# Optimization experiments

Hardware: AMD Instinct MI355X
Metric: run time of the kernel (lower is better)

## Reference

```python
import jax, jax.numpy as jnp
import numpy as np

B, T, H = 4, 4096, 1024


def setup_inputs() -> dict:
    key = jax.random.key(0)
    k1, k2 = jax.random.split(key)
    h = jax.random.normal(k1, (B, T, H), dtype=jnp.float32)
    # nn.Linear weight, scaled for stable magnitudes
    W = jax.random.normal(k2, (H, H), dtype=jnp.float32) / np.sqrt(H).astype(np.float32)
    return {"h": h, "W": W, "T_hist": 256}


def reference(h, W, T_hist):
    Bb, Tt, Hh = h.shape
    # K = Linear(h) = h @ W.T ; Q = V = h
    K = jnp.einsum('bth,oh->bto', h, W)
    scores = jnp.einsum('bqh,bkh->bqk', h, K) / jnp.sqrt(jnp.asarray(Hh, h.dtype))
    # banded mask: causal (j <= i) AND limited history (j >= i - (T_hist-1))
    i = jnp.arange(Tt)[:, None]
    j = jnp.arange(Tt)[None, :]
    valid = (j <= i) & (j >= i - (T_hist - 1))
    scores = jnp.where(valid[None, :, :], scores, -jnp.inf)
    attn = jax.nn.softmax(scores, axis=-1)
    attn = jnp.nan_to_num(attn, nan=0.0)  # matches torch nan_to_num(0.0)
    context = jnp.einsum('bqk,bkh->bqh', attn, h)
    return context
```

## Files before the change

### kernel.cpp

```cpp
#include <hip/hip_runtime.h>
#include <hip/hip_bf16.h>

#define B_ 4
#define T_ 4096
#define H_ 1024
#define WP2 320

typedef short  s16x8 __attribute__((ext_vector_type(8)));
typedef float  f32x4 __attribute__((ext_vector_type(4)));
typedef unsigned short u16;

static __device__ __forceinline__ u16 bf16rn(float f) {
  unsigned int u = __float_as_uint(f);
  u += 0x7fffu + ((u >> 16) & 1u);
  return (u16)(u >> 16);
}

static __device__ __forceinline__ void gl2lds16(const u16* g, u16* l) {
  __builtin_amdgcn_global_load_lds(
      (__attribute__((address_space(1))) void*)(g),
      (__attribute__((address_space(3))) void*)(l), 16, 0, 0);
}

__global__ __launch_bounds__(256) void k_convT(const float* __restrict__ h,
                                               u16* __restrict__ hb,
                                               u16* __restrict__ hbT) {
  __shared__ unsigned int tile32[64 * 33];
  const int b  = blockIdx.z;
  const int t0 = blockIdx.y * 64;
  const int c0 = blockIdx.x * 64;
  const int t  = threadIdx.x;
  {
    const int r  = t >> 2;
    const int cq = (t & 3) << 4;
    const size_t g = (size_t)(b * T_ + t0 + r) * H_ + c0 + cq;
    const f32x4* src = (const f32x4*)(h + g);
    u16 o[16];
#pragma unroll
    for (int v = 0; v < 4; ++v) {
      f32x4 x = src[v];
#pragma unroll
      for (int j = 0; j < 4; ++j) o[v * 4 + j] = bf16rn(x[j]);
    }
    s16x8 w0, w1;
#pragma unroll
    for (int j = 0; j < 8; ++j) { w0[j] = (short)o[j]; w1[j] = (short)o[8 + j]; }
    *(s16x8*)(hb + g)     = w0;
    *(s16x8*)(hb + g + 8) = w1;
#pragma unroll
    for (int i = 0; i < 8; ++i)
      tile32[r * 33 + (cq >> 1) + i] =
          (unsigned int)o[2 * i] | ((unsigned int)o[2 * i + 1] << 16);
  }
  __syncthreads();
  {
    const int fpair = t & 31;
    const int kq    = t >> 5;
    unsigned int v[8];
#pragma unroll
    for (int j = 0; j < 8; ++j) v[j] = tile32[(kq * 8 + j) * 33 + fpair];
    s16x8 w0, w1;
#pragma unroll
    for (int j = 0; j < 8; ++j) {
      w0[j] = (short)(v[j] & 0xffffu);
      w1[j] = (short)(v[j] >> 16);
    }
    const size_t o0 = (size_t)(b * H_ + c0 + 2 * fpair) * T_ + t0 + kq * 8;
    *(s16x8*)(hbT + o0)      = w0;
    *(s16x8*)(hbT + o0 + T_) = w1;
  }
}

__global__ __launch_bounds__(256) void k_convW(const float* __restrict__ src,
                                               u16* __restrict__ dst) {
  const int i = (blockIdx.x * 256 + threadIdx.x) * 8;
  f32x4 a = *(const f32x4*)(src + i);
  f32x4 b = *(const f32x4*)(src + i + 4);
  s16x8 w;
#pragma unroll
  for (int j = 0; j < 4; ++j) {
    w[j]     = (short)bf16rn(a[j]);
    w[4 + j] = (short)bf16rn(b[j]);
  }
  *(s16x8*)(dst + i) = w;
}

__global__ __launch_bounds__(256) void k_gemmK(const u16* __restrict__ hb,
                                               const u16* __restrict__ Wb,
                                               u16* __restrict__ Kb) {
  __shared__ __align__(16) u16 As[3][512 * 8];
  __shared__ __align__(16) u16 Bs[3][512 * 8];
  const int t = threadIdx.x;
  const int id  = blockIdx.y * gridDim.x + blockIdx.x;
  const int swz = (id & 7) * 128 + (id >> 3);
  const int row0 = (swz >> 3) * 128;
  const int col0 = (swz & 7) * 128;
  const int lane = t & 63, wv = t >> 6;
  const int wr = wv >> 1, wc = wv & 1;
  const int l15 = lane & 15, quad = lane >> 4;

  const int c0 = t, c1 = t + 256;
  const size_t gA0 = (size_t)(row0 + (c0 >> 2)) * H_ + (c0 & 3) * 8;
  const size_t gA1 = (size_t)(row0 + (c1 >> 2)) * H_ + (c1 & 3) * 8;
  const size_t gB0 = (size_t)(col0 + (c0 >> 2)) * H_ + (c0 & 3) * 8;
  const size_t gB1 = (size_t)(col0 + (c1 >> 2)) * H_ + (c1 & 3) * 8;

  f32x4 acc[4][4];
#pragma unroll
  for (int m = 0; m < 4; ++m)
#pragma unroll
    for (int n = 0; n < 4; ++n) acc[m][n] = (f32x4)0.0f;

  gl2lds16(hb + gA0, &As[0][c0 * 8]);
  gl2lds16(hb + gA1, &As[0][c1 * 8]);
  gl2lds16(Wb + gB0, &Bs[0][c0 * 8]);
  gl2lds16(Wb + gB1, &Bs[0][c1 * 8]);
  gl2lds16(hb + gA0 + 32, &As[1][c0 * 8]);
  gl2lds16(hb + gA1 + 32, &As[1][c1 * 8]);
  gl2lds16(Wb + gB0 + 32, &Bs[1][c0 * 8]);
  gl2lds16(Wb + gB1 + 32, &Bs[1][c1 * 8]);
  asm volatile("s_waitcnt vmcnt(4)" ::: "memory");
  __builtin_amdgcn_s_barrier();

#pragma unroll
  for (int kt = 0; kt < 32; ++kt) {
    if (kt + 2 < 32) {
      const int sn = (kt + 2) % 3;
      const int off = (kt + 2) * 32;
      gl2lds16(hb + gA0 + off, &As[sn][c0 * 8]);
      gl2lds16(hb + gA1 + off, &As[sn][c1 * 8]);
      gl2lds16(Wb + gB0 + off, &Bs[sn][c0 * 8]);
      gl2lds16(Wb + gB1 + off, &Bs[sn][c1 * 8]);
    }
    const int sc = kt % 3;
    s16x8 aF[4], bF[4];
#pragma unroll
    for (int mt = 0; mt < 4; ++mt)
      aF[mt] = *(const s16x8*)&As[sc][((wr * 64 + mt * 16 + l15) * 4 + quad) * 8];
#pragma unroll
    for (int nt = 0; nt < 4; ++nt)
      bF[nt] = *(const s16x8*)&Bs[sc][((wc * 64 + nt * 16 + l15) * 4 + quad) * 8];
#pragma unroll
    for (int mt = 0; mt < 4; ++mt)
#pragma unroll
      for (int nt = 0; nt < 4; ++nt)
        acc[mt][nt] = __builtin_amdgcn_mfma_f32_16x16x32_bf16(aF[mt], bF[nt],
                                                              acc[mt][nt], 0, 0, 0);
    if (kt + 1 < 32) {
      if (kt <= 29) asm volatile("s_waitcnt vmcnt(4)" ::: "memory");
      else          asm volatile("s_waitcnt vmcnt(0)" ::: "memory");
      __builtin_amdgcn_s_barrier();
    }
  }
#pragma unroll
  for (int mt = 0; mt < 4; ++mt)
#pragma unroll
    for (int nt = 0; nt < 4; ++nt)
#pragma unroll
      for (int r = 0; r < 4; ++r) {
        const int row = row0 + wr * 64 + mt * 16 + quad * 4 + r;
        const int col = col0 + wc * 64 + nt * 16 + l15;
        Kb[(size_t)row * H_ + col] = bf16rn(acc[mt][nt][r]);
      }
}

__global__ __launch_bounds__(512) void k_scores(const u16* __restrict__ hb,
                                                const u16* __restrict__ Kb,
                                                u16* __restrict__ P) {
  __shared__ __align__(16) u16 Ks[3][1280 * 8];
  __shared__ float Sred[2][4][16];
  const int t = threadIdx.x;
  const int wv = t >> 6, lane = t & 63;
  const int l15 = lane & 15, quad = lane >> 4;
  const int id  = blockIdx.x;
  const int swz = (id & 7) * 64 + (id >> 3);
  const int b  = swz >> 7;
  const int q0 = (swz & 127) * 32;
  const int qt = wv & 1;
  const int sub = wv >> 1;
  const int qt0 = q0 + qt * 16;
  const int ktbase = (sub == 0) ? 0 : (1 + sub * 4);
  const int nkt = (sub == 0) ? 5 : 4;

  const u16* st[3];
  int cid[3];
#pragma unroll
  for (int p = 0; p < 3; ++p) {
    int c = p * 512 + t;
    if (c > 1279) c = 1279;
    cid[p] = c;
    if (c < 1152) {
      const int m = c >> 6, lr = (c >> 2) & 15, qd = c & 3;
      int tok = q0 - 256 + m * 16 + lr;
      if (tok < 0) tok = 0;
      st[p] = Kb + (size_t)(b * T_ + tok) * H_ + qd * 8;
    } else {
      const int qc = c - 1152;
      const int r = qc >> 2, qd = qc & 3;
      st[p] = hb + (size_t)(b * T_ + q0 + r) * H_ + qd * 8;
    }
  }
  const bool w03 = (t < 256);

  f32x4 acc[5];
#pragma unroll
  for (int i = 0; i < 5; ++i) acc[i] = (f32x4)0.0f;

  gl2lds16(st[0], &Ks[0][cid[0] * 8]);
  gl2lds16(st[1], &Ks[0][cid[1] * 8]);
  if (w03) gl2lds16(st[2], &Ks[0][cid[2] * 8]);
  gl2lds16(st[0] + 32, &Ks[1][cid[0] * 8]);
  gl2lds16(st[1] + 32, &Ks[1][cid[1] * 8]);
  if (w03) gl2lds16(st[2] + 32, &Ks[1][cid[2] * 8]);
  if (w03) asm volatile("s_waitcnt vmcnt(3)" ::: "memory");
  else     asm volatile("s_waitcnt vmcnt(2)" ::: "memory");
  __builtin_amdgcn_s_barrier();

#pragma unroll
  for (int s = 0; s < 32; ++s) {
    if (s + 2 < 32) {
      const int sn = (s + 2) % 3;
      const int off = (s + 2) * 32;
      gl2lds16(st[0] + off, &Ks[sn][cid[0] * 8]);
      gl2lds16(st[1] + off, &Ks[sn][cid[1] * 8]);
      if (w03) gl2lds16(st[2] + off, &Ks[sn][cid[2] * 8]);
    }
    const int sc = s % 3;
    const s16x8 aQ =
        *(const s16x8*)&Ks[sc][(1152 + (qt * 16 + l15) * 4 + quad) * 8];
#pragma unroll
    for (int i = 0; i < 5; ++i) {
      if (i < nkt) {
        const int m = qt + ktbase + i;
        const s16x8 bK = *(const s16x8*)&Ks[sc][(m * 64 + l15 * 4 + quad) * 8];
        acc[i] = __builtin_amdgcn_mfma_f32_16x16x32_bf16(aQ, bK, acc[i], 0, 0, 0);
      }
    }
    if (s + 1 < 32) {
      if (s <= 29) {
        if (w03) asm volatile("s_waitcnt vmcnt(3)" ::: "memory");
        else     asm volatile("s_waitcnt vmcnt(2)" ::: "memory");
      } else {
        asm volatile("s_waitcnt vmcnt(0)" ::: "memory");
      }
      __builtin_amdgcn_s_barrier();
    }
  }

  const float scale = 0.03125f;
#pragma unroll
  for (int r = 0; r < 4; ++r) {
    const int q = qt0 + quad * 4 + r;
    float sum = 0.0f;
#pragma unroll
    for (int i = 0; i < 5; ++i) {
      if (i < nkt) {
        const int k = qt0 - 256 + (ktbase + i) * 16 + l15;
        const bool valid = (k >= 0) && (k <= q) && (k >= q - 255);
        const float p = valid ? __expf(acc[i][r] * scale) : 0.0f;
        acc[i][r] = p;
        sum += p;
      }
    }
    sum += __shfl_xor(sum, 1);
    sum += __shfl_xor(sum, 2);
    sum += __shfl_xor(sum, 4);
    sum += __shfl_xor(sum, 8);
    if (l15 == 0) Sred[qt][sub][quad * 4 + r] = sum;
  }
  __syncthreads();
  const int toff = ((q0 & 32) >> 4) + qt;
#pragma unroll
  for (int r = 0; r < 4; ++r) {
    const int q = qt0 + quad * 4 + r;
    const int row = quad * 4 + r;
    const float inv = 1.0f / (Sred[qt][0][row] + Sred[qt][1][row] +
                              Sred[qt][2][row] + Sred[qt][3][row]);
    u16* prow = P + (size_t)(b * T_ + q) * WP2;
#pragma unroll
    for (int i = 0; i < 5; ++i)
      if (i < nkt) prow[(toff + ktbase + i) * 16 + l15] = bf16rn(acc[i][r] * inv);
    if (sub == 0) {
#pragma unroll
      for (int z = 0; z < 3; ++z) {
        const int slot = (toff + 17 + z) % 20;
        prow[slot * 16 + l15] = 0;
      }
    }
  }
}

__global__ __launch_bounds__(512) void k_ctx(const u16* __restrict__ P,
                                             const u16* __restrict__ hbT,
                                             float* __restrict__ out) {
  __shared__ __align__(16) u16 Vs[3][1280 * 8];
  const int t = threadIdx.x;
  const int wv = t >> 6, lane = t & 63;
  const int l15 = lane & 15, quad = lane >> 4;
  const int id  = blockIdx.x;
  const int swz = (id & 7) * 64 + (id >> 3);
  const int fhalf = swz & 1;
  const int blk   = swz >> 1;
  const int b  = blk >> 6;
  const int q0 = (blk & 63) * 64;
  const int qtile = wv & 3, fh = wv >> 2;
  const int qt0 = q0 + qtile * 16;

  const u16* prow = P + (size_t)(b * T_ + qt0 + l15) * WP2 + quad * 8;
  s16x8 aP[10];
#pragma unroll
  for (int c = 0; c < 10; ++c) aP[c] = *(const s16x8*)(prow + c * 32);

  const int tok0 = q0 - 256;
  const u16* vst[3];
  int cid[3];
#pragma unroll
  for (int p = 0; p < 3; ++p) {
    int c = p * 512 + t;
    if (c > 1279) c = 1279;
    cid[p] = c;
    const int cg = c >> 7, ft = (c >> 6) & 1, lr = (c >> 2) & 15, qd = c & 3;
    const int fr = ft * 16 + lr;
    int tok = tok0 + (cg * 4 + qd) * 8;
    if (tok < 0) tok = 0;
    vst[p] = hbT + (size_t)(b * H_ + fr) * T_ + tok;
  }
  const bool w03 = (t < 256);
  const size_t fbase = (size_t)(fhalf * 512) * T_;
  const size_t fstep = (size_t)32 * T_;

  gl2lds16(vst[0] + fbase, &Vs[0][cid[0] * 8]);
  gl2lds16(vst[1] + fbase, &Vs[0][cid[1] * 8]);
  if (w03) gl2lds16(vst[2] + fbase, &Vs[0][cid[2] * 8]);
  gl2lds16(vst[0] + fbase + fstep, &Vs[1][cid[0] * 8]);
  gl2lds16(vst[1] + fbase + fstep, &Vs[1][cid[1] * 8]);
  if (w03) gl2lds16(vst[2] + fbase + fstep, &Vs[1][cid[2] * 8]);
  if (w03) asm volatile("s_waitcnt vmcnt(3)" ::: "memory");
  else     asm volatile("s_waitcnt vmcnt(2)" ::: "memory");
  __builtin_amdgcn_s_barrier();

#pragma unroll
  for (int g = 0; g < 16; ++g) {
    if (g + 2 < 16) {
      const int sn = (g + 2) % 3;
      const size_t off = fbase + (size_t)(g + 2) * fstep;
      gl2lds16(vst[0] + off, &Vs[sn][cid[0] * 8]);
      gl2lds16(vst[1] + off, &Vs[sn][cid[1] * 8]);
      if (w03) gl2lds16(vst[2] + off, &Vs[sn][cid[2] * 8]);
    }
    const int sc = g % 3;
    f32x4 acc = (f32x4)0.0f;
#pragma unroll
    for (int c = 0; c < 10; ++c) {
      const s16x8 bv =
          *(const s16x8*)&Vs[sc][(c * 128 + fh * 64 + l15 * 4 + quad) * 8];
      acc = __builtin_amdgcn_mfma_f32_16x16x32_bf16(aP[c], bv, acc, 0, 0, 0);
    }
    if (g + 1 < 16) {
      if (g <= 13) {
        if (w03) asm volatile("s_waitcnt vmcnt(7)" ::: "memory");
        else     asm volatile("s_waitcnt vmcnt(6)" ::: "memory");
      } else {
        asm volatile("s_waitcnt vmcnt(4)" ::: "memory");
      }
      __builtin_amdgcn_s_barrier();
    }
    const int f0 = (fhalf * 16 + g) * 32 + fh * 16 + l15;
#pragma unroll
    for (int r = 0; r < 4; ++r)
      out[(size_t)(b * T_ + qt0 + quad * 4 + r) * H_ + f0] = acc[r];
  }
}

extern "C" void kernel_launch(void* const* d_in, const int* in_sizes, int n_in,
                              void* d_out, int out_size, void* d_ws, size_t ws_size,
                              hipStream_t stream) {
  const float* h  = (const float*)d_in[0];
  const float* Wf = (const float*)d_in[1];

  char* ws = (char*)d_ws;
  u16* hb  = (u16*)(ws);
  u16* hbT = (u16*)(ws + (size_t)33554432);
  u16* Kb  = (u16*)(ws + (size_t)67108864);
  u16* Wb  = (u16*)(ws + (size_t)100663296);
  u16* P   = (u16*)(ws + (size_t)102760448);
  float* out = (float*)d_out;

  k_convT <<<dim3(H_ / 64, T_ / 64, B_), 256, 0, stream>>>(h, hb, hbT);
  k_convW <<<dim3(512), 256, 0, stream>>>(Wf, Wb);
  k_gemmK <<<dim3(H_ / 128, (B_ * T_) / 128), 256, 0, stream>>>(hb, Wb, Kb);
  k_scores<<<dim3((B_ * T_) / 32), 512, 0, stream>>>(hb, Kb, P);
  k_ctx   <<<dim3(2 * (B_ * T_) / 64), 512, 0, stream>>>(P, hbT, out);
}
```

Baseline: 221.4 us.

## Retile context kernel to 128-query blocks with shared V tiles across query pairs

The context kernel now has each block cover 128 queries and a quarter of the feature dimension. Each wave computes two 16-query tiles that share one V fragment from LDS, so V bytes loaded per output are reduced and the pipeline covers 8 feature groups instead of 16. The transpose kernel's write pattern is also changed so each thread writes full 8-token runs for one feature row, two halves 32 tokens apart, for more contiguous hbT stores. The trade-off is more registers for two sets of P fragments, a larger LDS buffer, and more careful vmcnt accounting.

```diff
diff --git a/kernel.cpp b/kernel.cpp
--- a/kernel.cpp
+++ b/kernel.cpp
@@ -54,20 +54,19 @@
   }
   __syncthreads();
   {
-    const int fpair = t & 31;
-    const int kq    = t >> 5;
-    unsigned int v[8];
-#pragma unroll
-    for (int j = 0; j < 8; ++j) v[j] = tile32[(kq * 8 + j) * 33 + fpair];
+    const int f    = t >> 2;
+    const int toct = t & 3;
+    const int dcol = f >> 1;
+    const int sh   = (f & 1) << 4;
     s16x8 w0, w1;
 #pragma unroll
     for (int j = 0; j < 8; ++j) {
-      w0[j] = (short)(v[j] & 0xffffu);
-      w1[j] = (short)(v[j] >> 16);
-    }
-    const size_t o0 = (size_t)(b * H_ + c0 + 2 * fpair) * T_ + t0 + kq * 8;
+      w0[j] = (short)((tile32[(toct * 8 + j) * 33 + dcol]      >> sh) & 0xffffu);
+      w1[j] = (short)((tile32[(32 + toct * 8 + j) * 33 + dcol] >> sh) & 0xffffu);
+    }
+    const size_t o0 = (size_t)(b * H_ + c0 + f) * T_ + t0 + toct * 8;
     *(s16x8*)(hbT + o0)      = w0;
-    *(s16x8*)(hbT + o0 + T_) = w1;
+    *(s16x8*)(hbT + o0 + 32) = w1;
   }
 }
 
@@ -290,85 +289,90 @@
   }
 }
 
-__global__ __launch_bounds__(512) void k_ctx(const u16* __restrict__ P,
-                                             const u16* __restrict__ hbT,
-                                             float* __restrict__ out) {
-  __shared__ __align__(16) u16 Vs[3][1280 * 8];
+__global__ __launch_bounds__(512, 4) void k_ctx(const u16* __restrict__ P,
+                                                const u16* __restrict__ hbT,
+                                                float* __restrict__ out) {
+  __shared__ __align__(16) u16 Vs[3][1536 * 8];
   const int t = threadIdx.x;
   const int wv = t >> 6, lane = t & 63;
   const int l15 = lane & 15, quad = lane >> 4;
   const int id  = blockIdx.x;
   const int swz = (id & 7) * 64 + (id >> 3);
-  const int fhalf = swz & 1;
-  const int blk   = swz >> 1;
-  const int b  = blk >> 6;
-  const int q0 = (blk & 63) * 64;
-  const int qtile = wv & 3, fh = wv >> 2;
-  const int qt0 = q0 + qtile * 16;
-
-  const u16* prow = P + (size_t)(b * T_ + qt0 + l15) * WP2 + quad * 8;
-  s16x8 aP[10];
-#pragma unroll
-  for (int c = 0; c < 10; ++c) aP[c] = *(const s16x8*)(prow + c * 32);
+  const int fq   = swz & 3;
+  const int qblk = swz >> 2;
+  const int b  = qblk >> 5;
+  const int q0 = (qblk & 31) * 128;
+  const int fh = wv & 1;
+  const int qp = wv >> 1;
+  const int ghalfoff = (qp >> 1) << 1;
+  const int qt0A = q0 + (qp * 2) * 16;
+  const int qt0B = q0 + (qp * 2 + 1) * 16;
+
+  const u16* prA = P + (size_t)(b * T_ + qt0A + l15) * WP2 + quad * 8;
+  const u16* prB = P + (size_t)(b * T_ + qt0B + l15) * WP2 + quad * 8;
+  s16x8 aPA[10], aPB[10];
+#pragma unroll
+  for (int c = 0; c < 10; ++c) {
+    aPA[c] = *(const s16x8*)(prA + c * 32);
+    aPB[c] = *(const s16x8*)(prB + c * 32);
+  }
+#pragma unroll
+  for (int c = 0; c < 10; ++c) {
+    asm volatile("" : "+v"(aPA[c]));
+    asm volatile("" : "+v"(aPB[c]));
+  }
 
   const int tok0 = q0 - 256;
   const u16* vst[3];
   int cid[3];
 #pragma unroll
   for (int p = 0; p < 3; ++p) {
-    int c = p * 512 + t;
-    if (c > 1279) c = 1279;
+    const int c = p * 512 + t;
     cid[p] = c;
     const int cg = c >> 7, ft = (c >> 6) & 1, lr = (c >> 2) & 15, qd = c & 3;
     const int fr = ft * 16 + lr;
     int tok = tok0 + (cg * 4 + qd) * 8;
     if (tok < 0) tok = 0;
-    vst[p] = hbT + (size_t)(b * H_ + fr) * T_ + tok;
-  }
-  const bool w03 = (t < 256);
-  const size_t fbase = (size_t)(fhalf * 512) * T_;
+    vst[p] = hbT + (size_t)(b * H_ + fq * 256 + fr) * T_ + tok;
+  }
   const size_t fstep = (size_t)32 * T_;
 
-  gl2lds16(vst[0] + fbase, &Vs[0][cid[0] * 8]);
-  gl2lds16(vst[1] + fbase, &Vs[0][cid[1] * 8]);
-  if (w03) gl2lds16(vst[2] + fbase, &Vs[0][cid[2] * 8]);
-  gl2lds16(vst[0] + fbase + fstep, &Vs[1][cid[0] * 8]);
-  gl2lds16(vst[1] + fbase + fstep, &Vs[1][cid[1] * 8]);
-  if (w03) gl2lds16(vst[2] + fbase + fstep, &Vs[1][cid[2] * 8]);
-  if (w03) asm volatile("s_waitcnt vmcnt(3)" ::: "memory");
-  else     asm volatile("s_waitcnt vmcnt(2)" ::: "memory");
+#pragma unroll
+  for (int p = 0; p < 3; ++p) gl2lds16(vst[p], &Vs[0][cid[p] * 8]);
+#pragma unroll
+  for (int p = 0; p < 3; ++p) gl2lds16(vst[p] + fstep, &Vs[1][cid[p] * 8]);
+  asm volatile("s_waitcnt vmcnt(3)" ::: "memory");
   __builtin_amdgcn_s_barrier();
 
 #pragma unroll
-  for (int g = 0; g < 16; ++g) {
-    if (g + 2 < 16) {
+  for (int g = 0; g < 8; ++g) {
+    if (g + 2 < 8) {
       const int sn = (g + 2) % 3;
-      const size_t off = fbase + (size_t)(g + 2) * fstep;
-      gl2lds16(vst[0] + off, &Vs[sn][cid[0] * 8]);
-      gl2lds16(vst[1] + off, &Vs[sn][cid[1] * 8]);
-      if (w03) gl2lds16(vst[2] + off, &Vs[sn][cid[2] * 8]);
+      const size_t off = (size_t)(g + 2) * fstep;
+#pragma unroll
+      for (int p = 0; p < 3; ++p) gl2lds16(vst[p] + off, &Vs[sn][cid[p] * 8]);
     }
     const int sc = g % 3;
-    f32x4 acc = (f32x4)0.0f;
+    f32x4 accA = (f32x4)0.0f, accB = (f32x4)0.0f;
 #pragma unroll
     for (int c = 0; c < 10; ++c) {
-      const s16x8 bv =
-          *(const s16x8*)&Vs[sc][(c * 128 + fh * 64 + l15 * 4 + quad) * 8];
-      acc = __builtin_amdgcn_mfma_f32_16x16x32_bf16(aP[c], bv, acc, 0, 0, 0);
-    }
-    if (g + 1 < 16) {
-      if (g <= 13) {
-        if (w03) asm volatile("s_waitcnt vmcnt(7)" ::: "memory");
-        else     asm volatile("s_waitcnt vmcnt(6)" ::: "memory");
-      } else {
-        asm volatile("s_waitcnt vmcnt(4)" ::: "memory");
-      }
+      const s16x8 bv = *(const s16x8*)
+          &Vs[sc][((c + ghalfoff) * 128 + fh * 64 + l15 * 4 + quad) * 8];
+      accA = __builtin_amdgcn_mfma_f32_16x16x32_bf16(aPA[c], bv, accA, 0, 0, 0);
+      accB = __builtin_amdgcn_mfma_f32_16x16x32_bf16(aPB[c], bv, accB, 0, 0, 0);
+    }
+    if (g + 1 < 8) {
+      if (g == 0)      asm volatile("s_waitcnt vmcnt(3)"  ::: "memory");
+      else if (g <= 5) asm volatile("s_waitcnt vmcnt(11)" ::: "memory");
+      else             asm volatile("s_waitcnt vmcnt(8)"  ::: "memory");
       __builtin_amdgcn_s_barrier();
     }
-    const int f0 = (fhalf * 16 + g) * 32 + fh * 16 + l15;
-#pragma unroll
-    for (int r = 0; r < 4; ++r)
-      out[(size_t)(b * T_ + qt0 + quad * 4 + r) * H_ + f0] = acc[r];
+    const int f0 = fq * 256 + g * 32 + fh * 16 + l15;
+#pragma unroll
+    for (int r = 0; r < 4; ++r) {
+      out[(size_t)(b * T_ + qt0A + quad * 4 + r) * H_ + f0] = accA[r];
+      out[(size_t)(b * T_ + qt0B + quad * 4 + r) * H_ + f0] = accB[r];
+    }
   }
 }
 
@@ -390,5 +394,5 @@
   k_convW <<<dim3(512), 256, 0, stream>>>(Wf, Wb);
   k_gemmK <<<dim3(H_ / 128, (B_ * T_) / 128), 256, 0, stream>>>(hb, Wb, Kb);
   k_scores<<<dim3((B_ * T_) / 32), 512, 0, stream>>>(hb, Kb, P);
-  k_ctx   <<<dim3(2 * (B_ * T_) / 64), 512, 0, stream>>>(P, hbT, out);
-}
+  k_ctx   <<<dim3(4 * (B_ * T_) / 128), 512, 0, stream>>>(P, hbT, out);
+}
```

Result: no change. 221.2 us (-0.1%).
